# Kernel optimization log

Hardware: AMD Instinct MI355X
Metric: run time of the kernel (lower is better)

## Reference

```python
import jax, jax.numpy as jnp
import numpy as np

VOCAB = 10000
X_DIM = 128
HID = 256


def setup_inputs() -> dict:
    key = jax.random.key(0)
    ks = jax.random.split(key, 8)
    B, S = 128, 50
    x = jax.random.randint(ks[0], (B, S), 0, VOCAB, dtype=jnp.int32).astype(jnp.int64)
    emb = jax.random.normal(ks[1], (VOCAB, X_DIM), dtype=jnp.float32) * 0.02
    # PyTorch nn.RNN params: W_ih [H, X], W_hh [H, H], b_ih [H], b_hh [H]
    W_ih = jax.random.normal(ks[2], (HID, X_DIM), dtype=jnp.float32) * (1.0 / np.sqrt(HID))
    W_hh = jax.random.normal(ks[3], (HID, HID), dtype=jnp.float32) * (1.0 / np.sqrt(HID))
    b_ih = jax.random.normal(ks[4], (HID,), dtype=jnp.float32) * 0.01
    b_hh = jax.random.normal(ks[5], (HID,), dtype=jnp.float32) * 0.01
    # nn.Linear: W_aff [V, H], b_aff [V]
    W_aff = jax.random.normal(ks[6], (VOCAB, HID), dtype=jnp.float32) * (1.0 / np.sqrt(HID))
    b_aff = jax.random.normal(ks[7], (VOCAB,), dtype=jnp.float32) * 0.01
    return {"x": x, "emb": emb, "W_ih": W_ih, "W_hh": W_hh,
            "b_ih": b_ih, "b_hh": b_hh, "W_aff": W_aff, "b_aff": b_aff}


def reference(x, emb, W_ih, W_hh, b_ih, b_hh, W_aff, b_aff):
    B, S = x.shape
    embs = emb[x]                                    # [B, S, X]
    # Precompute input projection for all timesteps (batched GEMM)
    xin = jnp.einsum('bsx,hx->bsh', embs, W_ih) + b_ih + b_hh  # [B, S, H]
    h0 = jnp.zeros((B, HID), dtype=embs.dtype)

    def step(h, xt):
        h = jnp.tanh(xt + h @ W_hh.T)
        return h, h

    _, hs = jax.lax.scan(step, h0, jnp.swapaxes(xin, 0, 1))  # hs: [S, B, H]
    hs = jnp.swapaxes(hs, 0, 1)                              # [B, S, H]
    ys = jnp.einsum('bsh,vh->bsv', hs, W_aff) + b_aff        # [B, S, V]
    return ys
```

## Files before the change

kernel.cpp:

```cpp
#include <hip/hip_runtime.h>
#include <hip/hip_bf16.h>
#include <stdint.h>

#define VOCAB 10000
#define XDIM 128
#define HID 256
#define BATCH 128
#define SEQ 50
#define ROWS (BATCH * SEQ)

#define BM 128
#define BN 256
#define BK 64
#define NTM 50
#define NTN 40

typedef __bf16 bf16x8 __attribute__((ext_vector_type(8)));
typedef float f32x4 __attribute__((ext_vector_type(4)));

__device__ __forceinline__ uint16_t f2bf(float f) {
    union { float f; uint32_t i; } v;
    v.f = f;
    uint32_t x = v.i;
    return (uint16_t)((x + 0x7fffu + ((x >> 16) & 1u)) >> 16);
}

__global__ __launch_bounds__(256) void k0_cast(
    const float* __restrict__ src, uint16_t* __restrict__ dst) {
    const int i = (blockIdx.x * 256 + threadIdx.x) * 8;
    float4 a = *(const float4*)(src + i);
    float4 b = *(const float4*)(src + i + 4);
    uint16_t t[8];
    t[0] = f2bf(a.x); t[1] = f2bf(a.y); t[2] = f2bf(a.z); t[3] = f2bf(a.w);
    t[4] = f2bf(b.x); t[5] = f2bf(b.y); t[6] = f2bf(b.z); t[7] = f2bf(b.w);
    *(uint4*)(dst + i) = *(const uint4*)t;
}

__global__ __launch_bounds__(256, 2) void k1_xin(
    const int* __restrict__ x, const float* __restrict__ emb,
    const float* __restrict__ Wih, const float* __restrict__ bih,
    const float* __restrict__ bhh, float* __restrict__ xin) {
    __shared__ __align__(16) float es[8][XDIM];
    const int r0 = blockIdx.x * 8;
    const int tid = threadIdx.x;

    {
        const int row = tid >> 5, c = tid & 31;
        const int tok = x[r0 + row];
        *(float4*)&es[row][c * 4] = *(const float4*)(emb + tok * XDIM + c * 4);
    }
    __syncthreads();

    const int j = tid;
    float wf[XDIM];
    const float4* wrow = (const float4*)(Wih + j * XDIM);
#pragma unroll
    for (int c = 0; c < 32; ++c) *(float4*)&wf[c * 4] = wrow[c];
    const float bias = bih[j] + bhh[j];

    float acc[8];
#pragma unroll
    for (int r = 0; r < 8; ++r) acc[r] = bias;
#pragma unroll
    for (int k4 = 0; k4 < 32; ++k4) {
#pragma unroll
        for (int r = 0; r < 8; ++r) {
            float4 e = *(const float4*)&es[r][k4 * 4];
            acc[r] += e.x * wf[k4 * 4 + 0] + e.y * wf[k4 * 4 + 1] +
                      e.z * wf[k4 * 4 + 2] + e.w * wf[k4 * 4 + 3];
        }
    }
#pragma unroll
    for (int r = 0; r < 8; ++r) xin[(r0 + r) * HID + j] = acc[r];
}

__global__ __launch_bounds__(512, 2) void k2_rnn(
    const float* __restrict__ xin, const float* __restrict__ Whh,
    uint16_t* __restrict__ hs) {
    __shared__ __align__(16) float hb[HID];
    __shared__ float ps[HID];
    const int b = blockIdx.x;
    const int j = threadIdx.x & 255;
    const int half = threadIdx.x >> 8;

    float wh[128];
    const float4* wrow = (const float4*)(Whh + j * HID + half * 128);
#pragma unroll
    for (int c = 0; c < 32; ++c) *(float4*)&wh[c * 4] = wrow[c];

    if (threadIdx.x < HID) hb[threadIdx.x] = 0.0f;
    __syncthreads();

    const float* xr = xin + b * SEQ * HID;
    uint16_t* hr = hs + b * SEQ * HID;

    for (int t = 0; t < SEQ; ++t) {
        const float xv = xr[t * HID + j];
        const float4* h4 = (const float4*)(hb + half * 128);
        float a0 = 0.f, a1 = 0.f, a2 = 0.f, a3 = 0.f;
#pragma unroll
        for (int c = 0; c < 32; ++c) {
            float4 v = h4[c];
            a0 += v.x * wh[c * 4 + 0];
            a1 += v.y * wh[c * 4 + 1];
            a2 += v.z * wh[c * 4 + 2];
            a3 += v.w * wh[c * 4 + 3];
        }
        const float part = (a0 + a1) + (a2 + a3);
        if (half) ps[j] = part;
        __syncthreads();
        if (!half) {
            const float hn = tanhf(part + ps[j] + xv);
            hb[j] = hn;
            hr[t * HID + j] = f2bf(hn);
        }
        __syncthreads();
    }
}

__global__ __launch_bounds__(256, 2) void k3_gemm(
    const uint16_t* __restrict__ A,
    const uint16_t* __restrict__ Bw,
    const float* __restrict__ baff,
    float* __restrict__ out) {
    __shared__ __align__(16) uint16_t As[BM * BK];
    __shared__ __align__(16) uint16_t Bs[BN * BK];

    const int bid = blockIdx.x;
    const int bm = bid % NTM, bn = bid / NTM;
    const int m0 = bm * BM, n0 = bn * BN;
    const int tid = threadIdx.x;
    const int wv = tid >> 6, ln = tid & 63;
    const int wm = wv & 1, wn = wv >> 1;
    const int quad = ln >> 4, l15 = ln & 15;

    f32x4 acc[4][8];
#pragma unroll
    for (int i = 0; i < 4; ++i)
#pragma unroll
        for (int jj = 0; jj < 8; ++jj) acc[i][jj] = (f32x4)0.0f;

    const int lrow = ln >> 3;
    const int gsw = ((ln & 7) ^ lrow) * 8;

    for (int kt = 0; kt < 4; ++kt) {
        const int k0 = kt * BK;
#pragma unroll
        for (int i = 0; i < 4; ++i) {
            const int ci = wv * 4 + i;
            const uint16_t* g = A + (size_t)(m0 + ci * 8 + lrow) * HID + k0 + gsw;
            __builtin_amdgcn_global_load_lds(
                (const __attribute__((address_space(1))) void*)g,
                (__attribute__((address_space(3))) void*)(As + ci * 512), 16, 0, 0);
        }
#pragma unroll
        for (int i = 0; i < 8; ++i) {
            const int ci = wv * 8 + i;
            int n = n0 + ci * 8 + lrow;
            if (n > VOCAB - 1) n = VOCAB - 1;
            const uint16_t* g = Bw + (size_t)n * HID + k0 + gsw;
            __builtin_amdgcn_global_load_lds(
                (const __attribute__((address_space(1))) void*)g,
                (__attribute__((address_space(3))) void*)(Bs + ci * 512), 16, 0, 0);
        }
        __syncthreads();

#pragma unroll
        for (int kk = 0; kk < 2; ++kk) {
            const int gk = kk * 4 + quad;
            bf16x8 af[4], bf[8];
#pragma unroll
            for (int tm = 0; tm < 4; ++tm) {
                const int R = wm * 64 + tm * 16 + l15;
                af[tm] = *(const bf16x8*)&As[R * 64 + ((gk ^ (R & 7)) * 8)];
            }
#pragma unroll
            for (int tn = 0; tn < 8; ++tn) {
                const int R = wn * 128 + tn * 16 + l15;
                bf[tn] = *(const bf16x8*)&Bs[R * 64 + ((gk ^ (R & 7)) * 8)];
            }
#pragma unroll
            for (int tm = 0; tm < 4; ++tm)
#pragma unroll
                for (int tn = 0; tn < 8; ++tn)
                    acc[tm][tn] = __builtin_amdgcn_mfma_f32_16x16x32_bf16(
                        af[tm], bf[tn], acc[tm][tn], 0, 0, 0);
        }
        __syncthreads();
    }

    float bias[8];
#pragma unroll
    for (int tn = 0; tn < 8; ++tn) {
        int n = n0 + wn * 128 + tn * 16 + l15;
        bias[tn] = baff[n > VOCAB - 1 ? VOCAB - 1 : n];
    }
#pragma unroll
    for (int tm = 0; tm < 4; ++tm) {
        const int mbase = m0 + wm * 64 + tm * 16 + quad * 4;
#pragma unroll
        for (int r = 0; r < 4; ++r) {
            float* orow = out + (size_t)(mbase + r) * VOCAB;
#pragma unroll
            for (int tn = 0; tn < 8; ++tn) {
                int n = n0 + wn * 128 + tn * 16 + l15;
                if (n < VOCAB) orow[n] = acc[tm][tn][r] + bias[tn];
            }
        }
    }
}

extern "C" void kernel_launch(void* const* d_in, const int* in_sizes, int n_in,
                              void* d_out, int out_size, void* d_ws, size_t ws_size,
                              hipStream_t stream) {
    const int* x = (const int*)d_in[0];
    const float* emb = (const float*)d_in[1];
    const float* Wih = (const float*)d_in[2];
    const float* Whh = (const float*)d_in[3];
    const float* bih = (const float*)d_in[4];
    const float* bhh = (const float*)d_in[5];
    const float* Waff = (const float*)d_in[6];
    const float* baff = (const float*)d_in[7];

    float* xin = (float*)d_ws;
    uint16_t* hsb = (uint16_t*)((char*)d_ws + (size_t)ROWS * HID * 4);
    uint16_t* Wb = hsb + (size_t)ROWS * HID;
    float* out = (float*)d_out;

    k0_cast<<<(VOCAB * HID) / (256 * 8), 256, 0, stream>>>(Waff, Wb);
    k1_xin<<<ROWS / 8, 256, 0, stream>>>(x, emb, Wih, bih, bhh, xin);
    k2_rnn<<<BATCH, 512, 0, stream>>>(xin, Whh, hsb);
    k3_gemm<<<NTM * NTN, 256, 0, stream>>>(hsb, Wb, baff, out);
}
```

Measured before the change: 384.7 us.

## Load GEMM fragments directly from global, remap block order, nontemporal output stores

The output GEMM no longer stages A and B tiles through LDS. Each lane now loads its bf16x8 MFMA fragments straight from global memory (relying on L2/L1 reuse), which removes the shared-memory staging and the __syncthreads barriers. The block index is remapped so that consecutive blocks fall into eight interleaved groups, which changes L2 locality across M and N tiles. Output writes use nontemporal stores to avoid polluting the cache with the large logits array. The risk is redundant global traffic and uncoalesced 16-byte row-strided loads replacing the cooperative LDS loads.

New measurement: 445.3 us. 15.8% more time.

```diff
diff --git a/kernel.cpp b/kernel.cpp
--- a/kernel.cpp
+++ b/kernel.cpp
@@ -11,7 +11,6 @@
 
 #define BM 128
 #define BN 256
-#define BK 64
 #define NTM 50
 #define NTN 40
 
@@ -123,10 +122,8 @@
     const uint16_t* __restrict__ Bw,
     const float* __restrict__ baff,
     float* __restrict__ out) {
-    __shared__ __align__(16) uint16_t As[BM * BK];
-    __shared__ __align__(16) uint16_t Bs[BN * BK];
-
-    const int bid = blockIdx.x;
+    const int bid0 = blockIdx.x;
+    const int bid = (bid0 & 7) * ((NTM * NTN) / 8) + (bid0 >> 3);
     const int bm = bid % NTM, bn = bid / NTM;
     const int m0 = bm * BM, n0 = bn * BN;
     const int tid = threadIdx.x;
@@ -140,53 +137,33 @@
 #pragma unroll
         for (int jj = 0; jj < 8; ++jj) acc[i][jj] = (f32x4)0.0f;
 
-    const int lrow = ln >> 3;
-    const int gsw = ((ln & 7) ^ lrow) * 8;
-
-    for (int kt = 0; kt < 4; ++kt) {
-        const int k0 = kt * BK;
-#pragma unroll
-        for (int i = 0; i < 4; ++i) {
-            const int ci = wv * 4 + i;
-            const uint16_t* g = A + (size_t)(m0 + ci * 8 + lrow) * HID + k0 + gsw;
-            __builtin_amdgcn_global_load_lds(
-                (const __attribute__((address_space(1))) void*)g,
-                (__attribute__((address_space(3))) void*)(As + ci * 512), 16, 0, 0);
-        }
-#pragma unroll
-        for (int i = 0; i < 8; ++i) {
-            const int ci = wv * 8 + i;
-            int n = n0 + ci * 8 + lrow;
-            if (n > VOCAB - 1) n = VOCAB - 1;
-            const uint16_t* g = Bw + (size_t)n * HID + k0 + gsw;
-            __builtin_amdgcn_global_load_lds(
-                (const __attribute__((address_space(1))) void*)g,
-                (__attribute__((address_space(3))) void*)(Bs + ci * 512), 16, 0, 0);
-        }
-        __syncthreads();
-
-#pragma unroll
-        for (int kk = 0; kk < 2; ++kk) {
-            const int gk = kk * 4 + quad;
-            bf16x8 af[4], bf[8];
-#pragma unroll
-            for (int tm = 0; tm < 4; ++tm) {
-                const int R = wm * 64 + tm * 16 + l15;
-                af[tm] = *(const bf16x8*)&As[R * 64 + ((gk ^ (R & 7)) * 8)];
-            }
-#pragma unroll
-            for (int tn = 0; tn < 8; ++tn) {
-                const int R = wn * 128 + tn * 16 + l15;
-                bf[tn] = *(const bf16x8*)&Bs[R * 64 + ((gk ^ (R & 7)) * 8)];
-            }
-#pragma unroll
-            for (int tm = 0; tm < 4; ++tm)
-#pragma unroll
-                for (int tn = 0; tn < 8; ++tn)
-                    acc[tm][tn] = __builtin_amdgcn_mfma_f32_16x16x32_bf16(
-                        af[tm], bf[tn], acc[tm][tn], 0, 0, 0);
-        }
-        __syncthreads();
+    const uint16_t* ab[4];
+#pragma unroll
+    for (int tm = 0; tm < 4; ++tm)
+        ab[tm] = A + (size_t)(m0 + wm * 64 + tm * 16 + l15) * HID + quad * 8;
+    const uint16_t* bb[8];
+#pragma unroll
+    for (int tn = 0; tn < 8; ++tn) {
+        int n = n0 + wn * 128 + tn * 16 + l15;
+        if (n > VOCAB - 1) n = VOCAB - 1;
+        bb[tn] = Bw + (size_t)n * HID + quad * 8;
+    }
+
+#pragma unroll
+    for (int ks = 0; ks < 8; ++ks) {
+        bf16x8 af[4], bf[8];
+#pragma unroll
+        for (int tm = 0; tm < 4; ++tm)
+            af[tm] = *(const bf16x8*)(ab[tm] + ks * 32);
+#pragma unroll
+        for (int tn = 0; tn < 8; ++tn)
+            bf[tn] = *(const bf16x8*)(bb[tn] + ks * 32);
+#pragma unroll
+        for (int tm = 0; tm < 4; ++tm)
+#pragma unroll
+            for (int tn = 0; tn < 8; ++tn)
+                acc[tm][tn] = __builtin_amdgcn_mfma_f32_16x16x32_bf16(
+                    af[tm], bf[tn], acc[tm][tn], 0, 0, 0);
     }
 
     float bias[8];
@@ -203,8 +180,10 @@
             float* orow = out + (size_t)(mbase + r) * VOCAB;
 #pragma unroll
             for (int tn = 0; tn < 8; ++tn) {
-                int n = n0 + wn * 128 + tn * 16 + l15;
-                if (n < VOCAB) orow[n] = acc[tm][tn][r] + bias[tn];
+                const int n = n0 + wn * 128 + tn * 16 + l15;
+                if (n < VOCAB)
+                    __builtin_nontemporal_store(acc[tm][tn][r] + bias[tn],
+                                                &orow[n]);
             }
         }
     }
```

## Stage GEMM output through LDS for vectorized nontemporal stores and swizzle block order

Applied to the files above, without the earlier changes.

The output-projection GEMM epilogue now writes each 16x128 accumulator tile into padded shared memory and reads it back as contiguous float4 rows. It then issues 16-byte nontemporal global stores instead of scattered scalar stores. The block index is also remapped so consecutive blocks cover different tiles, which changes cache locality. The goal is to cut write-transaction overhead on the large 6400x10000 fp32 output, at the cost of extra LDS traffic and barriers in the epilogue. VOCAB is divisible by 4, so the gn<VOCAB guard on float4 stores stays correct.

New measurement: 363.4 us. 1.06x faster.

```diff
diff --git a/kernel.cpp b/kernel.cpp
--- a/kernel.cpp
+++ b/kernel.cpp
@@ -123,10 +123,12 @@
     const uint16_t* __restrict__ Bw,
     const float* __restrict__ baff,
     float* __restrict__ out) {
-    __shared__ __align__(16) uint16_t As[BM * BK];
-    __shared__ __align__(16) uint16_t Bs[BN * BK];
-
-    const int bid = blockIdx.x;
+    __shared__ __align__(16) char smem[49152];
+    uint16_t* As = (uint16_t*)smem;
+    uint16_t* Bs = (uint16_t*)(smem + BM * BK * 2);
+
+    const int bid0 = blockIdx.x;
+    const int bid = (bid0 & 7) * ((NTM * NTN) / 8) + (bid0 >> 3);
     const int bm = bid % NTM, bn = bid / NTM;
     const int m0 = bm * BM, n0 = bn * BN;
     const int tid = threadIdx.x;
@@ -189,6 +191,7 @@
         __syncthreads();
     }
 
+    float* csw = (float*)smem + wv * 16 * 132;
     float bias[8];
 #pragma unroll
     for (int tn = 0; tn < 8; ++tn) {
@@ -197,16 +200,25 @@
     }
 #pragma unroll
     for (int tm = 0; tm < 4; ++tm) {
-        const int mbase = m0 + wm * 64 + tm * 16 + quad * 4;
-#pragma unroll
-        for (int r = 0; r < 4; ++r) {
-            float* orow = out + (size_t)(mbase + r) * VOCAB;
-#pragma unroll
-            for (int tn = 0; tn < 8; ++tn) {
-                int n = n0 + wn * 128 + tn * 16 + l15;
-                if (n < VOCAB) orow[n] = acc[tm][tn][r] + bias[tn];
-            }
-        }
+#pragma unroll
+        for (int tn = 0; tn < 8; ++tn)
+#pragma unroll
+            for (int r = 0; r < 4; ++r)
+                csw[(quad * 4 + r) * 132 + tn * 16 + l15] =
+                    acc[tm][tn][r] + bias[tn];
+        __syncthreads();
+#pragma unroll
+        for (int it = 0; it < 8; ++it) {
+            const int row = it * 2 + (ln >> 5);
+            const int c4 = (ln & 31) * 4;
+            const f32x4 v = *(const f32x4*)&csw[row * 132 + c4];
+            const int gm = m0 + wm * 64 + tm * 16 + row;
+            const int gn = n0 + wn * 128 + c4;
+            if (gn < VOCAB)
+                __builtin_nontemporal_store(
+                    v, (f32x4*)(out + (size_t)gm * VOCAB + gn));
+        }
+        __syncthreads();
     }
 }
 
```
